# Kernel optimization log

Hardware: AMD Instinct MI355X
Metric: run time of the kernel (lower is better)

Reference implementation:

```python
import jax, jax.numpy as jnp
import numpy as np

B, CI, HW, K, C, NH, L = 512, 3, 28, 28 // 28 and 0 or 7, 1024, 16, 12
K = 7


def setup_inputs() -> dict:
    key = jax.random.key(0)
    ks = jax.random.split(key, 8)
    s = 0.02
    return {
        "x": jax.random.normal(ks[0], (B, CI, HW, HW), jnp.float32),
        "conv_w": jax.random.normal(ks[1], (C, CI, K, K), jnp.float32) * s,  # Conv2d weight [Co,Ci,k,k], shared with deconv
        "ln1_w": jnp.ones((L, C), jnp.float32),
        "ln1_b": jnp.zeros((L, C), jnp.float32),
        "wq": jax.random.normal(ks[2], (L, C, C), jnp.float32) * s,
        "wk": jax.random.normal(ks[3], (L, C, C), jnp.float32) * s,
        "wv": jax.random.normal(ks[4], (L, C, C), jnp.float32) * s,
        "ln2_w": jnp.ones((L, C), jnp.float32),
        "ln2_b": jnp.zeros((L, C), jnp.float32),
        "mlp_w": jax.random.normal(ks[5], (L, C, C), jnp.float32) * s,
        "mlp_b": jnp.zeros((L, C), jnp.float32),
        "out_w": jax.random.normal(ks[6], (C, C), jnp.float32) * s,
        "out_b": jnp.zeros((C,), jnp.float32),
        "head_num": NH,
    }


def _layernorm(x, w, b, eps=1e-5):
    m = jnp.mean(x, axis=-1, keepdims=True)
    v = jnp.var(x, axis=-1, keepdims=True)  # biased var, matches torch LayerNorm
    return (x - m) * jax.lax.rsqrt(v + eps) * w + b


def _attn(h, wq, wk, wv, nh):
    b, t, c = h.shape
    hd = c // nh
    q = (h @ wq.T).reshape(b, t, nh, hd).transpose(0, 2, 1, 3)  # [B,H,T,hd]
    k = (h @ wk.T).reshape(b, t, nh, hd).transpose(0, 2, 1, 3)
    v = (h @ wv.T).reshape(b, t, nh, hd).transpose(0, 2, 1, 3)
    scores = jnp.einsum("bhqd,bhkd->bhqk", q, k) / jnp.sqrt(jnp.float32(hd))
    mask = jnp.tril(jnp.ones((t, t), bool))
    scores = jnp.where(mask, scores, -jnp.inf)
    a = jax.nn.softmax(scores, axis=-1)
    o = jnp.einsum("bhqk,bhkd->bhqd", a, v)
    return o.transpose(0, 2, 1, 3).reshape(b, t, c)


def _forward(x, conv_w, ln1_w, ln1_b, wq, wk, wv, ln2_w, ln2_b, mlp_w, mlp_b, out_w, out_b, head_num):
    b, ci, hh, ww = x.shape
    co, _, k, _ = conv_w.shape
    # thumbnail: bilinear downsample to (k,k) (align_corners=False == half-pixel), then k-strided conv -> [B,Co]
    thumb = jax.image.resize(x, (b, ci, k, k), method="bilinear", antialias=False)
    thumb_tok = jnp.einsum("bcpq,dcpq->bd", thumb, conv_w)
    # kernel==stride conv == patchify + matmul
    hp, wp = hh // k, ww // k
    xp = x.reshape(b, ci, hp, k, wp, k)
    patches = jnp.einsum("bcipjq,dcpq->bdij", xp, conv_w).reshape(b, co, hp * wp)
    h = jnp.concatenate([thumb_tok[:, :, None], patches], axis=-1).transpose(0, 2, 1)  # [B,T=1+hp*wp,C]
    nlayers = ln1_w.shape[0]
    for l in range(nlayers):
        a = _attn(_layernorm(h, ln1_w[l], ln1_b[l]), wq[l], wk[l], wv[l], head_num)
        h = h + a
        m = _layernorm(h, ln2_w[l], ln2_b[l]) @ mlp_w[l].T + mlp_b[l]
        h = h + m
    logits = h @ out_w.T + out_b  # [B,T,C]
    # decode: ConvTranspose2d(kernel=stride=k) with shared weight; input [B,Co,1,T] -> [B,Ci,k,T*k]
    z = logits.transpose(0, 2, 1)  # [B,Co,T]
    t = z.shape[-1]
    out = jnp.einsum("bcs,cdhw->bdhsw", z, conv_w).reshape(b, ci, k, t * k)
    return out


def reference(x, conv_w, ln1_w, ln1_b, wq, wk, wv, ln2_w, ln2_b, mlp_w, mlp_b, out_w, out_b, head_num):
    return _forward(x, conv_w, ln1_w, ln1_b, wq, wk, wv, ln2_w, ln2_b, mlp_w, mlp_b, out_w, out_b, head_num)
```

## Files before the change

### kernel.cpp

```cpp
#include <hip/hip_runtime.h>


typedef unsigned short u16;
typedef short bfrag8 __attribute__((ext_vector_type(8)));
typedef float facc4 __attribute__((ext_vector_type(4)));

__device__ __forceinline__ u16 f2bf(float f) {
  union { float f; unsigned u; } x; x.f = f;
  unsigned r = x.u + 0x7fffu + ((x.u >> 16) & 1u);
  return (u16)(r >> 16);
}
__device__ __forceinline__ float bf2f(u16 h) {
  union { unsigned u; float f; } x; x.u = ((unsigned)h) << 16;
  return x.f;
}


template <int MODE>
__global__ __launch_bounds__(512, 2) void gemm256(
    const u16* __restrict__ A, int lda,
    const u16* __restrict__ B0, const u16* __restrict__ B1, const u16* __restrict__ B2,
    int ldb, int K, int cpx,
    void* __restrict__ outp, long long zstride, int ldo,
    const float* __restrict__ bias)
{
  __shared__ u16 S[49152];

  const int bid = blockIdx.x;
  const int wg = (bid & 7) * cpx + (bid >> 3);
  const int perz = 34 * 4;
  const int z = wg / perz;
  const int r0 = wg - z * perz;
  const int y = r0 >> 2;
  const int x = r0 & 3;
  const int m0 = y * 256, n0 = x * 256;
  const u16* __restrict__ B = (z == 0) ? B0 : ((z == 1) ? B1 : B2);

  const int tid = threadIdx.x;
  const int wave = tid >> 6;
  const int lane = tid & 63;
  const int lrow = lane & 15, lquad = lane >> 4;
  const int mh = wave >> 2;
  const int w4 = wave & 3;
  const int wm = mh * 128, wn = w4 * 64;

  int offA[4], offB[2];
#pragma unroll
  for (int im = 0; im < 4; ++im) {
    const int rr = mh * 64 + im * 16 + lrow;
    const int l = rr >> 1;
    const int s = (lquad + 4 * (rr & 1)) ^ (l & 7);
    offA[im] = l * 64 + s * 8;
  }
#pragma unroll
  for (int in = 0; in < 2; ++in) {
    const int rr = w4 * 32 + in * 16 + lrow;
    const int l = rr >> 1;
    const int s = (lquad + 4 * (rr & 1)) ^ (l & 7);
    offB[in] = l * 64 + s * 8;
  }

  const int rgn = wave >> 1;
  const int hh = wave & 1;
  const u16* gsrc[4];
  int gdst[4];
#pragma unroll
  for (int i = 0; i < 4; ++i) {
    const int p = hh * 256 + i * 64 + lane;
    const int l = p >> 3, s = p & 7;
    const int v = s ^ (l & 7);
    const int rrs = 2 * l + (v >> 2);
    const int cs = v & 3;
    if (rgn < 2) {
      const int grow = m0 + (rrs >> 6) * 128 + rgn * 64 + (rrs & 63);
      gsrc[i] = A + (long long)grow * lda + cs * 8;
    } else {
      const int gcol = n0 + (rrs >> 5) * 64 + (rgn - 2) * 32 + (rrs & 31);
      gsrc[i] = B + (long long)gcol * ldb + cs * 8;
    }
    gdst[i] = rgn * 4096 + p * 8;
  }

  facc4 acc[8][4] = {};

#pragma unroll
  for (int i = 0; i < 4; ++i) {
    __builtin_amdgcn_global_load_lds((const __attribute__((address_space(1))) void*)gsrc[i],
                                     (__attribute__((address_space(3))) void*)(S + gdst[i]), 16, 0, 0);
    gsrc[i] += 32;
  }
#pragma unroll
  for (int i = 0; i < 4; ++i) {
    __builtin_amdgcn_global_load_lds((const __attribute__((address_space(1))) void*)gsrc[i],
                                     (__attribute__((address_space(3))) void*)(S + 16384 + gdst[i]), 16, 0, 0);
    gsrc[i] += 32;
  }
  asm volatile("s_waitcnt vmcnt(4)" ::: "memory");
  __builtin_amdgcn_sched_barrier(0);
  __builtin_amdgcn_s_barrier();
  __builtin_amdgcn_sched_barrier(0);

  const int NT = K >> 5;
  int sb0 = 0, sb1 = 16384, sb2 = 32768;

  for (int t = 0; t < NT; ++t) {
    bfrag8 a0[4], a1[4], bf0[2], bf1[2];
#pragma unroll
    for (int im = 0; im < 4; ++im) a0[im] = *(const bfrag8*)&S[sb0 + offA[im]];
#pragma unroll
    for (int in = 0; in < 2; ++in) bf0[in] = *(const bfrag8*)&S[sb0 + 8192 + offB[in]];
#pragma unroll
    for (int in = 0; in < 2; ++in) bf1[in] = *(const bfrag8*)&S[sb0 + 12288 + offB[in]];
#pragma unroll
    for (int im = 0; im < 4; ++im) a1[im] = *(const bfrag8*)&S[sb0 + 4096 + offA[im]];
    if (t + 2 < NT) {
#pragma unroll
      for (int i = 0; i < 4; ++i) {
        __builtin_amdgcn_global_load_lds((const __attribute__((address_space(1))) void*)gsrc[i],
                                         (__attribute__((address_space(3))) void*)(S + sb2 + gdst[i]), 16, 0, 0);
        gsrc[i] += 32;
      }
    }
    __builtin_amdgcn_s_setprio(1);
#pragma unroll
    for (int im = 0; im < 4; ++im)
#pragma unroll
      for (int in = 0; in < 2; ++in)
        acc[im][in] = __builtin_amdgcn_mfma_f32_16x16x32_bf16(a0[im], bf0[in], acc[im][in], 0, 0, 0);
#pragma unroll
    for (int im = 0; im < 4; ++im)
#pragma unroll
      for (int in = 0; in < 2; ++in)
        acc[im][2 + in] = __builtin_amdgcn_mfma_f32_16x16x32_bf16(a0[im], bf1[in], acc[im][2 + in], 0, 0, 0);
#pragma unroll
    for (int im = 0; im < 4; ++im)
#pragma unroll
      for (int in = 0; in < 2; ++in)
        acc[4 + im][2 + in] = __builtin_amdgcn_mfma_f32_16x16x32_bf16(a1[im], bf1[in], acc[4 + im][2 + in], 0, 0, 0);
#pragma unroll
    for (int im = 0; im < 4; ++im)
#pragma unroll
      for (int in = 0; in < 2; ++in)
        acc[4 + im][in] = __builtin_amdgcn_mfma_f32_16x16x32_bf16(a1[im], bf0[in], acc[4 + im][in], 0, 0, 0);
    __builtin_amdgcn_s_setprio(0);

    if (t + 1 < NT) {
      __builtin_amdgcn_sched_barrier(0);
      if (t + 2 < NT) asm volatile("s_waitcnt vmcnt(4)" ::: "memory");
      else            asm volatile("s_waitcnt vmcnt(0)" ::: "memory");
      __builtin_amdgcn_sched_barrier(0);
      __builtin_amdgcn_s_barrier();
      __builtin_amdgcn_sched_barrier(0);
    }
    const int tmp = sb0; sb0 = sb1; sb1 = sb2; sb2 = tmp;
  }

#pragma unroll
  for (int in = 0; in < 4; ++in) {
    const int col = n0 + wn + in * 16 + lrow;
    const float bb = bias ? bias[col] : 0.0f;
#pragma unroll
    for (int im = 0; im < 8; ++im) {
#pragma unroll
      for (int r = 0; r < 4; ++r) {
        const int row = m0 + wm + im * 16 + lquad * 4 + r;
        const float v = acc[im][in][r] + bb;
        if (MODE == 1) {
          (((u16*)outp) + zstride * z)[(long long)row * ldo + col] = f2bf(v);
        } else if (MODE == 2) {
          ((float*)outp)[(long long)row * ldo + col] += v;
        } else {
          const long long off = (long long)row * ldo + col;
          const float nv = ((float*)outp)[off] + v;
          ((float*)outp)[off] = nv;
          ((u16*)zstride)[off] = f2bf(nv);
        }
      }
    }
  }
}

template <int MODE>
__global__ __launch_bounds__(256) void gemm_bt(
    const u16* __restrict__ A, int lda,
    const u16* __restrict__ B0, const u16* __restrict__ B1, const u16* __restrict__ B2,
    int ldb, int K, int NX,
    void* __restrict__ outp, long long zstride, int ldo,
    const float* __restrict__ bias)
{
  __shared__ __align__(16) u16 As[8192];
  __shared__ __align__(16) u16 Bs[8192];

  const int l = blockIdx.x;
  const int xcd = l & 7;
  const int j = l >> 3;
  const int per_epoch = 9 * NX;
  const int z = j / per_epoch;
  const int r2 = j - z * per_epoch;
  const int g = r2 / NX;
  const int y = xcd + 8 * g;
  if (y >= 68) return;
  const int x = r2 - g * NX;
  const int n0 = x * 128;
  const int m0 = y * 128;
  const u16* __restrict__ B = (z == 0) ? B0 : ((z == 1) ? B1 : B2);

  const int tid  = threadIdx.x;
  const int wave = tid >> 6;
  const int lane = tid & 63;
  const int wm   = (wave >> 1) * 64;
  const int wn   = (wave & 1) * 64;
  const int lrow = lane & 15;
  const int lquad = lane >> 4;

  facc4 acc[4][4] = {};

  const u16* ga[4]; const u16* gb[4];
#pragma unroll
  for (int j2 = 0; j2 < 4; ++j2) {
    const int s = tid + 256 * j2;
    const int t = s >> 9, s2 = s & 511;
    const int r = s2 >> 2, c = (s2 & 3) + 4 * t;
    ga[j2] = A + (long long)(m0 + r) * lda + c * 8;
    gb[j2] = B + (long long)(n0 + r) * ldb + c * 8;
  }

  const int aoff = (wm + lrow) * 32 + lquad * 8;
  const int boff = (wn + lrow) * 32 + lquad * 8;

  for (int k0 = 0; k0 < K; k0 += 64) {
#pragma unroll
    for (int j2 = 0; j2 < 4; ++j2) {
      __builtin_amdgcn_global_load_lds((const __attribute__((address_space(1))) void*)ga[j2],
                                       (__attribute__((address_space(3))) void*)(As + (tid + 256 * j2) * 8), 16, 0, 0);
      __builtin_amdgcn_global_load_lds((const __attribute__((address_space(1))) void*)gb[j2],
                                       (__attribute__((address_space(3))) void*)(Bs + (tid + 256 * j2) * 8), 16, 0, 0);
      ga[j2] += 64; gb[j2] += 64;
    }
    __syncthreads();

#pragma unroll
    for (int t = 0; t < 2; ++t) {
      bfrag8 af[4], bfr[4];
#pragma unroll
      for (int im = 0; im < 4; ++im) af[im] = *(const bfrag8*)(As + t * 4096 + aoff + 512 * im);
#pragma unroll
      for (int in = 0; in < 4; ++in) bfr[in] = *(const bfrag8*)(Bs + t * 4096 + boff + 512 * in);
#pragma unroll
      for (int im = 0; im < 4; ++im)
#pragma unroll
        for (int in = 0; in < 4; ++in)
          acc[im][in] = __builtin_amdgcn_mfma_f32_16x16x32_bf16(af[im], bfr[in], acc[im][in], 0, 0, 0);
    }
    __syncthreads();
  }

#pragma unroll
  for (int in = 0; in < 4; ++in) {
    const int col = n0 + wn + in * 16 + lrow;
    const float bb = bias ? bias[col] : 0.0f;
#pragma unroll
    for (int im = 0; im < 4; ++im) {
#pragma unroll
      for (int r = 0; r < 4; ++r) {
        const int row = m0 + wm + im * 16 + lquad * 4 + r;
        const float v = acc[im][in][r] + bb;
        if (MODE == 0) {
          ((float*)outp)[(long long)row * ldo + col] = v;
        } else if (MODE == 1) {
          (((u16*)outp) + zstride * z)[(long long)row * ldo + col] = f2bf(v);
        } else if (MODE == 2) {
          ((float*)outp)[(long long)row * ldo + col] += v;
        } else if (MODE == 4) {
          const long long off = (long long)row * ldo + col;
          const float nv = ((float*)outp)[off] + v;
          ((float*)outp)[off] = nv;
          ((u16*)zstride)[off] = f2bf(nv);
        } else {
          if (col < 147) {
            const int b = row / 17, s = row - b * 17;
            const int d = col / 49, rem = col - d * 49;
            const int hk = rem / 7, wk = rem - hk * 7;
            ((float*)outp)[(long long)((b * 3 + d) * 7 + hk) * 119 + s * 7 + wk] = v;
          }
        }
      }
    }
  }
}

__global__ __launch_bounds__(256) void ln_kernel(
    const float* __restrict__ h, const float* __restrict__ w,
    const float* __restrict__ b, u16* __restrict__ out)
{
  const long long row = blockIdx.x;
  const int t = threadIdx.x;
  const float4 v = ((const float4*)(h + row * 1024))[t];
  float s = v.x + v.y + v.z + v.w;
  float q = v.x * v.x + v.y * v.y + v.z * v.z + v.w * v.w;
  for (int o = 32; o > 0; o >>= 1) { s += __shfl_down(s, o); q += __shfl_down(q, o); }
  __shared__ float ss[4], sq[4];
  const int wave = t >> 6, lane = t & 63;
  if (lane == 0) { ss[wave] = s; sq[wave] = q; }
  __syncthreads();
  const float st = ss[0] + ss[1] + ss[2] + ss[3];
  const float qt = sq[0] + sq[1] + sq[2] + sq[3];
  const float mean = st * (1.0f / 1024.0f);
  const float var = qt * (1.0f / 1024.0f) - mean * mean;
  const float inv = rsqrtf(var + 1e-5f);
  const float4 w4 = ((const float4*)w)[t];
  const float4 b4 = ((const float4*)b)[t];
  ushort4 o;
  o.x = f2bf((v.x - mean) * inv * w4.x + b4.x);
  o.y = f2bf((v.y - mean) * inv * w4.y + b4.y);
  o.z = f2bf((v.z - mean) * inv * w4.z + b4.z);
  o.w = f2bf((v.w - mean) * inv * w4.w + b4.w);
  ((ushort4*)(out + row * 1024))[t] = o;
}

__global__ __launch_bounds__(256) void attn_kernel(const u16* __restrict__ QKV,
                                                   float* __restrict__ h)
{
  const int blk = blockIdx.x;
  const int b = blk >> 4, head = blk & 15;
  __shared__ float qs[17][64], ks[17][64], vs[17][64];
  __shared__ float sc[17][20];
  const long long base = (long long)b * 17408 + head * 64;
  const u16* Q  = QKV;
  const u16* Kp = QKV + 8912896LL;
  const u16* V  = QKV + 17825792LL;
  const int tid = threadIdx.x;

  if (tid < 136) {
    const int t = tid >> 3, dg = (tid & 7) * 8;
    const long long off = base + (long long)t * 1024 + dg;
    union { uint4 u; u16 s[8]; } xq, xk, xv;
    xq.u = *(const uint4*)(Q + off);
    xk.u = *(const uint4*)(Kp + off);
    xv.u = *(const uint4*)(V + off);
#pragma unroll
    for (int j = 0; j < 8; ++j) {
      qs[t][dg + j] = bf2f(xq.s[j]);
      ks[t][dg + j] = bf2f(xk.s[j]);
      vs[t][dg + j] = bf2f(xv.s[j]);
    }
  }
  __syncthreads();

  for (int i = tid; i < 289; i += 256) {
    const int tq = i / 17, tk = i % 17;
    float a = 0.0f;
    if (tk <= tq) {
#pragma unroll
      for (int d = 0; d < 64; ++d) a += qs[tq][d] * ks[tk][d];
      a *= 0.125f;
    }
    sc[tq][tk] = a;
  }
  __syncthreads();

  if (tid < 17) {
    const int tq = tid;
    float m = -1e30f;
    for (int tk = 0; tk <= tq; ++tk) m = fmaxf(m, sc[tq][tk]);
    float s = 0.0f;
    for (int tk = 0; tk <= tq; ++tk) { const float e = __expf(sc[tq][tk] - m); sc[tq][tk] = e; s += e; }
    const float inv = 1.0f / s;
    for (int tk = 0; tk <= tq; ++tk) sc[tq][tk] *= inv;
  }
  __syncthreads();

  for (int i = tid; i < 272; i += 256) {
    const int tq = i >> 4, dg = (i & 15) * 4;
    float o0 = 0, o1 = 0, o2 = 0, o3 = 0;
    for (int tk = 0; tk <= tq; ++tk) {
      const float s = sc[tq][tk];
      o0 += s * vs[tk][dg];     o1 += s * vs[tk][dg + 1];
      o2 += s * vs[tk][dg + 2]; o3 += s * vs[tk][dg + 3];
    }
    float4* hp = (float4*)(h + base + (long long)tq * 1024 + dg);
    float4 hv = *hp;
    hv.x += o0; hv.y += o1; hv.z += o2; hv.w += o3;
    *hp = hv;
  }
}

__global__ void build_p(const float* __restrict__ x, u16* __restrict__ P)
{
  const int n = blockIdx.x;
  const int j = threadIdx.x;
  if (j >= 192) return;
  const int b = n / 17, t = n % 17;
  float val = 0.0f;
  if (j < 147) {
    const int c = j / 49, rem = j % 49, p = rem / 7, q = rem % 7;
    const float* xb = x + (long long)(b * 3 + c) * 784;
    if (t == 0) {
      const int r = 4 * p + 1, cc = 4 * q + 1;
      val = 0.25f * (xb[r * 28 + cc] + xb[r * 28 + cc + 1] +
                     xb[(r + 1) * 28 + cc] + xb[(r + 1) * 28 + cc + 1]);
    } else {
      const int s = t - 1, ii = s >> 2, jj = s & 3;
      val = xb[(7 * ii + p) * 28 + 7 * jj + q];
    }
  }
  P[(long long)n * 192 + j] = f2bf(val);
}

__global__ __launch_bounds__(256) void cvt_conv(const float* __restrict__ cw,
                                                u16* __restrict__ Wc, u16* __restrict__ cw2)
{
  const int i = blockIdx.x * 256 + threadIdx.x;
  if (i < 196608) {
    const int d = i / 192, j = i % 192;
    Wc[i] = (j < 147) ? f2bf(cw[d * 147 + j]) : (u16)0;
  } else {
    const int i2 = i - 196608;
    if (i2 < 262144) {
      const int j = i2 / 1024, c = i2 % 1024;
      cw2[i2] = (j < 147) ? f2bf(cw[c * 147 + j]) : (u16)0;
    }
  }
}

__global__ __launch_bounds__(256) void wprime_kernel(
    const u16* __restrict__ cw2, const float* __restrict__ outw,
    u16* __restrict__ Wp)
{
  const int k = blockIdx.x * 256 + threadIdx.x;
  const int j = blockIdx.y;
  float a = 0.0f;
  for (int c = 0; c < 1024; ++c)
    a += bf2f(cw2[j * 1024 + c]) * outw[c * 1024 + k];
  Wp[j * 1024 + k] = f2bf(a);
}

__global__ __launch_bounds__(256) void bprime_kernel(
    const u16* __restrict__ cw2, const float* __restrict__ outb,
    float* __restrict__ bp)
{
  const int j = threadIdx.x;
  float a = 0.0f;
  for (int c = 0; c < 1024; ++c) a += outb[c] * bf2f(cw2[j * 1024 + c]);
  bp[j] = a;
}

__global__ __launch_bounds__(256) void cvt_all(
    const float* __restrict__ wq, const float* __restrict__ wk,
    const float* __restrict__ wv, const float* __restrict__ mlpw,
    const float* __restrict__ outw, u16* __restrict__ wAll)
{
  const int i = blockIdx.x * 256 + threadIdx.x;
  const int which = i >> 18;
  const int off = i & 262143;
  const float4* src;
  if (which < 48) {
    const int layer = which >> 2, sub = which & 3;
    const float* base = (sub == 0) ? wq : (sub == 1) ? wk : (sub == 2) ? wv : mlpw;
    src = (const float4*)(base + (size_t)layer * 1048576) + off;
  } else {
    src = (const float4*)outw + off;
  }
  const float4 v = *src;
  ushort4 o; o.x = f2bf(v.x); o.y = f2bf(v.y); o.z = f2bf(v.z); o.w = f2bf(v.w);
  *(ushort4*)(wAll + (size_t)which * 1048576 + (size_t)off * 4) = o;
}

__global__ __launch_bounds__(256) void cvt4(const float* __restrict__ a0, const float* __restrict__ a1,
                                            const float* __restrict__ a2, const float* __restrict__ a3,
                                            u16* __restrict__ o3, u16* __restrict__ om)
{
  const int i = blockIdx.x * 256 + threadIdx.x;
  const int which = i >> 20, off = i & 1048575;
  const float* src = (which == 0) ? a0 : (which == 1) ? a1 : (which == 2) ? a2 : a3;
  const float v = src[off];
  if (which < 3) o3[which * 1048576 + off] = f2bf(v);
  else           om[off] = f2bf(v);
}

__global__ __launch_bounds__(256) void cvtN(const float* __restrict__ in, u16* __restrict__ out, int n)
{
  const int i = blockIdx.x * 256 + threadIdx.x;
  if (i < n) out[i] = f2bf(in[i]);
}

extern "C" void kernel_launch(void* const* d_in, const int* in_sizes, int n_in,
                              void* d_out, int out_size, void* d_ws, size_t ws_size,
                              hipStream_t stream)
{
  const float* x     = (const float*)d_in[0];
  const float* convw = (const float*)d_in[1];
  const float* ln1w  = (const float*)d_in[2];
  const float* ln1b  = (const float*)d_in[3];
  const float* wq    = (const float*)d_in[4];
  const float* wk    = (const float*)d_in[5];
  const float* wv    = (const float*)d_in[6];
  const float* ln2w  = (const float*)d_in[7];
  const float* ln2b  = (const float*)d_in[8];
  const float* mlpw  = (const float*)d_in[9];
  const float* mlpb  = (const float*)d_in[10];
  const float* outw  = (const float*)d_in[11];
  const float* outb  = (const float*)d_in[12];

  char* w = (char*)d_ws;
  const bool big = (ws_size >= 214500352ULL);

  const int G_QKV = 8 * 3 * 9 * 8;
  const int G_ONE = 8 * 1 * 9 * 8;
  const int G_DEC = 8 * 1 * 9 * 2;

  if (big) {
    float* h   = (float*)(w);
    u16* Abuf  = (u16*)(w + 35651584);
    u16* QKV   = (u16*)(w + 53477376);
    u16* wAll  = (u16*)(w + 106954752);
    u16* Wc    = (u16*)(w + 209715200);
    u16* cw2   = (u16*)(w + 210108416);
    u16* P     = (u16*)(w + 210632704);
    u16* Wp    = (u16*)(w + 213975040);
    float* bp  = (float*)(w + 214499328);

    cvt_all<<<50176, 256, 0, stream>>>(wq, wk, wv, mlpw, outw, wAll);
    cvt_conv<<<1792, 256, 0, stream>>>(convw, Wc, cw2);
    wprime_kernel<<<dim3(4, 256), 256, 0, stream>>>(cw2, outw, Wp);
    bprime_kernel<<<1, 256, 0, stream>>>(cw2, outb, bp);
    build_p<<<8704, 192, 0, stream>>>(x, P);
    gemm_bt<0><<<G_ONE, 256, 0, stream>>>(P, 192, Wc, Wc, Wc, 192, 192, 8,
                                          (void*)h, 0LL, 1024, nullptr);
    for (int l = 0; l < 12; ++l) {
      u16* wl = wAll + (size_t)l * 4194304;
      ln_kernel<<<8704, 256, 0, stream>>>(h, ln1w + l * 1024, ln1b + l * 1024, Abuf);
      gemm256<1><<<408, 512, 0, stream>>>(Abuf, 1024, wl, wl + 1048576, wl + 2097152,
                                          1024, 1024, 51, (void*)QKV, 8912896LL, 1024, nullptr);
      attn_kernel<<<8192, 256, 0, stream>>>(QKV, h);
      ln_kernel<<<8704, 256, 0, stream>>>(h, ln2w + l * 1024, ln2b + l * 1024, Abuf);
      if (l < 11) {
        gemm_bt<2><<<G_ONE, 256, 0, stream>>>(Abuf, 1024, wl + 3145728, wl, wl,
                                              1024, 1024, 8, (void*)h, 0LL, 1024, mlpb + l * 1024);
      } else {
        gemm_bt<4><<<G_ONE, 256, 0, stream>>>(Abuf, 1024, wl + 3145728, wl, wl,
                                              1024, 1024, 8, (void*)h,
                                              (long long)(uintptr_t)QKV, 1024,
                                              mlpb + l * 1024);
      }
    }
    gemm_bt<3><<<G_DEC, 256, 0, stream>>>(QKV, 1024, Wp, Wp, Wp,
                                          1024, 1024, 2, d_out, 0LL, 0, bp);
  } else {
    if (ws_size < 119603200ULL) return;
    float* h   = (float*)(w);
    u16* Abuf  = (u16*)(w + 35651584);
    u16* QKV   = (u16*)(w + 53477376);
    u16* wb3   = (u16*)(w + 106954752);
    u16* wmb   = (u16*)(w + 113246208);
    u16* Wc    = (u16*)(w + 115343360);
    u16* cw2   = (u16*)(w + 115736576);
    u16* P     = (u16*)(w + 116260864);

    cvt_conv<<<1792, 256, 0, stream>>>(convw, Wc, cw2);
    build_p<<<8704, 192, 0, stream>>>(x, P);
    gemm_bt<0><<<G_ONE, 256, 0, stream>>>(P, 192, Wc, Wc, Wc, 192, 192, 8,
                                          (void*)h, 0LL, 1024, nullptr);
    for (int l = 0; l < 12; ++l) {
      const size_t wo = (size_t)l * 1048576;
      cvt4<<<16384, 256, 0, stream>>>(wq + wo, wk + wo, wv + wo, mlpw + wo, wb3, wmb);
      ln_kernel<<<8704, 256, 0, stream>>>(h, ln1w + l * 1024, ln1b + l * 1024, Abuf);
      gemm_bt<1><<<G_QKV, 256, 0, stream>>>(Abuf, 1024, wb3, wb3 + 1048576, wb3 + 2097152,
                                            1024, 1024, 8, (void*)QKV, 8912896LL, 1024, nullptr);
      attn_kernel<<<8192, 256, 0, stream>>>(QKV, h);
      ln_kernel<<<8704, 256, 0, stream>>>(h, ln2w + l * 1024, ln2b + l * 1024, Abuf);
      gemm_bt<2><<<G_ONE, 256, 0, stream>>>(Abuf, 1024, wmb, wmb, wmb,
                                            1024, 1024, 8, (void*)h, 0LL, 1024, mlpb + l * 1024);
    }
    cvtN<<<34816, 256, 0, stream>>>(h, Abuf, 8912896);
    cvtN<<<4096, 256, 0, stream>>>(outw, wmb, 1048576);
    gemm_bt<1><<<G_ONE, 256, 0, stream>>>(Abuf, 1024, wmb, wmb, wmb,
                                          1024, 1024, 8, (void*)QKV, 0LL, 1024, outb);
    gemm_bt<3><<<G_DEC, 256, 0, stream>>>(QKV, 1024, cw2, cw2, cw2,
                                          1024, 1024, 2, d_out, 0LL, 0, nullptr);
  }
}
```

Measured before the change: 2.681 ms.

## Double-buffer gemm256 with register prefetch and route MLP GEMM through it

The gemm256 main loop moves from a three-stage LDS ring to two LDS buffers. Fragments for the next k-step are prefetched into a second register set while the current MFMAs run, and the loop is unrolled by two to swap register sets. The MLP projection (modes 2 and 4) now uses the 256x256 gemm256 kernel with 136 blocks instead of gemm_bt. This cuts LDS use and may allow more overlap, but it raises register pressure and forces a full vmcnt(0) wait each iteration. With only 136 blocks the MLP GEMM may also leave many CUs idle.

```diff
diff --git a/kernel.cpp b/kernel.cpp
--- a/kernel.cpp
+++ b/kernel.cpp
@@ -15,6 +15,49 @@
   return x.f;
 }
 
+
+#define GEMM256_MFMA_GROUPS(CA0, CA1, CB0, CB1)                                          \
+  __builtin_amdgcn_s_setprio(1);                                                         \
+  _Pragma("unroll") for (int im = 0; im < 4; ++im)                                       \
+    _Pragma("unroll") for (int in = 0; in < 2; ++in)                                     \
+      acc[im][in] = __builtin_amdgcn_mfma_f32_16x16x32_bf16(CA0[im], CB0[in], acc[im][in], 0, 0, 0); \
+  _Pragma("unroll") for (int im = 0; im < 4; ++im)                                       \
+    _Pragma("unroll") for (int in = 0; in < 2; ++in)                                     \
+      acc[im][2 + in] = __builtin_amdgcn_mfma_f32_16x16x32_bf16(CA0[im], CB1[in], acc[im][2 + in], 0, 0, 0); \
+  _Pragma("unroll") for (int im = 0; im < 4; ++im)                                       \
+    _Pragma("unroll") for (int in = 0; in < 2; ++in)                                     \
+      acc[4 + im][2 + in] = __builtin_amdgcn_mfma_f32_16x16x32_bf16(CA1[im], CB1[in], acc[4 + im][2 + in], 0, 0, 0); \
+  _Pragma("unroll") for (int im = 0; im < 4; ++im)                                       \
+    _Pragma("unroll") for (int in = 0; in < 2; ++in)                                     \
+      acc[4 + im][in] = __builtin_amdgcn_mfma_f32_16x16x32_bf16(CA1[im], CB0[in], acc[4 + im][in], 0, 0, 0); \
+  __builtin_amdgcn_s_setprio(0);
+
+#define GITER(TT, CA0, CA1, CB0, CB1, NA0, NA1, NB0, NB1)                                \
+  do {                                                                                   \
+    const int tt_ = (TT);                                                                \
+    if (tt_ + 1 < NT) {                                                                  \
+      const int sbR = ((tt_ + 1) & 1) << 14;                                             \
+      _Pragma("unroll") for (int im = 0; im < 4; ++im) NA0[im] = *(const bfrag8*)&S[sbR + offA[im]]; \
+      _Pragma("unroll") for (int in = 0; in < 2; ++in) NB0[in] = *(const bfrag8*)&S[sbR + 8192 + offB[in]]; \
+      _Pragma("unroll") for (int in = 0; in < 2; ++in) NB1[in] = *(const bfrag8*)&S[sbR + 12288 + offB[in]]; \
+      _Pragma("unroll") for (int im = 0; im < 4; ++im) NA1[im] = *(const bfrag8*)&S[sbR + 4096 + offA[im]]; \
+    }                                                                                    \
+    if (tt_ + 2 < NT) {                                                                  \
+      const int sbW = (tt_ & 1) << 14;                                                   \
+      _Pragma("unroll") for (int i = 0; i < 4; ++i)                                      \
+        __builtin_amdgcn_global_load_lds(                                                \
+            (const __attribute__((address_space(1))) void*)(gsrc[i] + (tt_ + 2) * 32),   \
+            (__attribute__((address_space(3))) void*)(S + sbW + gdst[i]), 16, 0, 0);     \
+    }                                                                                    \
+    GEMM256_MFMA_GROUPS(CA0, CA1, CB0, CB1)                                              \
+    if (tt_ + 1 < NT) {                                                                  \
+      __builtin_amdgcn_sched_barrier(0);                                                 \
+      asm volatile("s_waitcnt vmcnt(0) lgkmcnt(0)" ::: "memory");                        \
+      __builtin_amdgcn_sched_barrier(0);                                                 \
+      __builtin_amdgcn_s_barrier();                                                      \
+      __builtin_amdgcn_sched_barrier(0);                                                 \
+    }                                                                                    \
+  } while (0)
 
 template <int MODE>
 __global__ __launch_bounds__(512, 2) void gemm256(
@@ -24,7 +67,7 @@
     void* __restrict__ outp, long long zstride, int ldo,
     const float* __restrict__ bias)
 {
-  __shared__ u16 S[49152];
+  __shared__ u16 S[32768];
 
   const int bid = blockIdx.x;
   const int wg = (bid & 7) * cpx + (bid >> 3);
@@ -82,77 +125,40 @@
   }
 
   facc4 acc[8][4] = {};
-
-#pragma unroll
-  for (int i = 0; i < 4; ++i) {
-    __builtin_amdgcn_global_load_lds((const __attribute__((address_space(1))) void*)gsrc[i],
+  const int NT = K >> 5;
+
+#pragma unroll
+  for (int i = 0; i < 4; ++i)
+    __builtin_amdgcn_global_load_lds((const __attribute__((address_space(1))) void*)(gsrc[i]),
                                      (__attribute__((address_space(3))) void*)(S + gdst[i]), 16, 0, 0);
-    gsrc[i] += 32;
-  }
-#pragma unroll
-  for (int i = 0; i < 4; ++i) {
-    __builtin_amdgcn_global_load_lds((const __attribute__((address_space(1))) void*)gsrc[i],
+#pragma unroll
+  for (int i = 0; i < 4; ++i)
+    __builtin_amdgcn_global_load_lds((const __attribute__((address_space(1))) void*)(gsrc[i] + 32),
                                      (__attribute__((address_space(3))) void*)(S + 16384 + gdst[i]), 16, 0, 0);
-    gsrc[i] += 32;
-  }
-  asm volatile("s_waitcnt vmcnt(4)" ::: "memory");
+  asm volatile("s_waitcnt vmcnt(0)" ::: "memory");
   __builtin_amdgcn_sched_barrier(0);
   __builtin_amdgcn_s_barrier();
   __builtin_amdgcn_sched_barrier(0);
 
-  const int NT = K >> 5;
-  int sb0 = 0, sb1 = 16384, sb2 = 32768;
-
-  for (int t = 0; t < NT; ++t) {
-    bfrag8 a0[4], a1[4], bf0[2], bf1[2];
-#pragma unroll
-    for (int im = 0; im < 4; ++im) a0[im] = *(const bfrag8*)&S[sb0 + offA[im]];
-#pragma unroll
-    for (int in = 0; in < 2; ++in) bf0[in] = *(const bfrag8*)&S[sb0 + 8192 + offB[in]];
-#pragma unroll
-    for (int in = 0; in < 2; ++in) bf1[in] = *(const bfrag8*)&S[sb0 + 12288 + offB[in]];
-#pragma unroll
-    for (int im = 0; im < 4; ++im) a1[im] = *(const bfrag8*)&S[sb0 + 4096 + offA[im]];
-    if (t + 2 < NT) {
-#pragma unroll
-      for (int i = 0; i < 4; ++i) {
-        __builtin_amdgcn_global_load_lds((const __attribute__((address_space(1))) void*)gsrc[i],
-                                         (__attribute__((address_space(3))) void*)(S + sb2 + gdst[i]), 16, 0, 0);
-        gsrc[i] += 32;
-      }
-    }
-    __builtin_amdgcn_s_setprio(1);
-#pragma unroll
-    for (int im = 0; im < 4; ++im)
-#pragma unroll
-      for (int in = 0; in < 2; ++in)
-        acc[im][in] = __builtin_amdgcn_mfma_f32_16x16x32_bf16(a0[im], bf0[in], acc[im][in], 0, 0, 0);
-#pragma unroll
-    for (int im = 0; im < 4; ++im)
-#pragma unroll
-      for (int in = 0; in < 2; ++in)
-        acc[im][2 + in] = __builtin_amdgcn_mfma_f32_16x16x32_bf16(a0[im], bf1[in], acc[im][2 + in], 0, 0, 0);
-#pragma unroll
-    for (int im = 0; im < 4; ++im)
-#pragma unroll
-      for (int in = 0; in < 2; ++in)
-        acc[4 + im][2 + in] = __builtin_amdgcn_mfma_f32_16x16x32_bf16(a1[im], bf1[in], acc[4 + im][2 + in], 0, 0, 0);
-#pragma unroll
-    for (int im = 0; im < 4; ++im)
-#pragma unroll
-      for (int in = 0; in < 2; ++in)
-        acc[4 + im][in] = __builtin_amdgcn_mfma_f32_16x16x32_bf16(a1[im], bf0[in], acc[4 + im][in], 0, 0, 0);
-    __builtin_amdgcn_s_setprio(0);
-
-    if (t + 1 < NT) {
-      __builtin_amdgcn_sched_barrier(0);
-      if (t + 2 < NT) asm volatile("s_waitcnt vmcnt(4)" ::: "memory");
-      else            asm volatile("s_waitcnt vmcnt(0)" ::: "memory");
-      __builtin_amdgcn_sched_barrier(0);
-      __builtin_amdgcn_s_barrier();
-      __builtin_amdgcn_sched_barrier(0);
-    }
-    const int tmp = sb0; sb0 = sb1; sb1 = sb2; sb2 = tmp;
+  bfrag8 cA0[4], cA1[4], cB0[2], cB1[2];
+  bfrag8 nA0[4], nA1[4], nB0[2], nB1[2];
+#pragma unroll
+  for (int im = 0; im < 4; ++im) cA0[im] = *(const bfrag8*)&S[offA[im]];
+#pragma unroll
+  for (int in = 0; in < 2; ++in) cB0[in] = *(const bfrag8*)&S[8192 + offB[in]];
+#pragma unroll
+  for (int in = 0; in < 2; ++in) cB1[in] = *(const bfrag8*)&S[12288 + offB[in]];
+#pragma unroll
+  for (int im = 0; im < 4; ++im) cA1[im] = *(const bfrag8*)&S[4096 + offA[im]];
+  __builtin_amdgcn_sched_barrier(0);
+  asm volatile("s_waitcnt lgkmcnt(0)" ::: "memory");
+  __builtin_amdgcn_sched_barrier(0);
+  __builtin_amdgcn_s_barrier();
+  __builtin_amdgcn_sched_barrier(0);
+
+  for (int t = 0; t < NT; t += 2) {
+    GITER(t,     cA0, cA1, cB0, cB1, nA0, nA1, nB0, nB1);
+    GITER(t + 1, nA0, nA1, nB0, nB1, cA0, cA1, cB0, cB1);
   }
 
 #pragma unroll
@@ -535,13 +541,13 @@
       attn_kernel<<<8192, 256, 0, stream>>>(QKV, h);
       ln_kernel<<<8704, 256, 0, stream>>>(h, ln2w + l * 1024, ln2b + l * 1024, Abuf);
       if (l < 11) {
-        gemm_bt<2><<<G_ONE, 256, 0, stream>>>(Abuf, 1024, wl + 3145728, wl, wl,
-                                              1024, 1024, 8, (void*)h, 0LL, 1024, mlpb + l * 1024);
+        gemm256<2><<<136, 512, 0, stream>>>(Abuf, 1024, wl + 3145728, wl + 3145728, wl + 3145728,
+                                            1024, 1024, 17, (void*)h, 0LL, 1024, mlpb + l * 1024);
       } else {
-        gemm_bt<4><<<G_ONE, 256, 0, stream>>>(Abuf, 1024, wl + 3145728, wl, wl,
-                                              1024, 1024, 8, (void*)h,
-                                              (long long)(uintptr_t)QKV, 1024,
-                                              mlpb + l * 1024);
+        gemm256<4><<<136, 512, 0, stream>>>(Abuf, 1024, wl + 3145728, wl + 3145728, wl + 3145728,
+                                            1024, 1024, 17, (void*)h,
+                                            (long long)(uintptr_t)QKV, 1024,
+                                            mlpb + l * 1024);
       }
     }
     gemm_bt<3><<<G_DEC, 256, 0, stream>>>(QKV, 1024, Wp, Wp, Wp,
```

After: 2.892 ms. 1.08x slower.
